# Kernel tuning notes

Measured on AMD Instinct MI355X. Metric: run time of the kernel, lower is better.

The kernel has to match this reference:

```python
import jax, jax.numpy as jnp
import numpy as np

E = 512      # embedding_dim == head_dim
H = 8        # num_heads
F = E * H    # ffn_dim = 4096
B = 2
S = 2048
SCALE = float(np.sqrt(E))


def setup_inputs() -> dict:
    key = jax.random.key(0)
    kx, kq, kk, kv, ko = jax.random.split(key, 5)
    x = jax.random.normal(kx, (B, S, E), dtype=jnp.float32)
    # torch Linear weights: [out_features, in_features], y = x @ W.T
    w_std = 1.0 / np.sqrt(E)
    Wq = jax.random.normal(kq, (F, E), dtype=jnp.float32) * w_std
    Wk = jax.random.normal(kk, (F, E), dtype=jnp.float32) * w_std
    Wv = jax.random.normal(kv, (F, E), dtype=jnp.float32) * w_std
    Wo = jax.random.normal(ko, (E, F), dtype=jnp.float32) * (1.0 / np.sqrt(F))
    # causal mask: 1 where attended, 0 where masked (masked_fill(mask == 0, -inf))
    attn_mask = jnp.tril(jnp.ones((S, S), dtype=jnp.int32))[None, None]  # [1,1,S,S]
    return {"x": x, "attn_mask": attn_mask, "Wq": Wq, "Wk": Wk, "Wv": Wv, "Wo": Wo}


def reference(x, attn_mask, Wq, Wk, Wv, Wo):
    b, s, _ = x.shape
    # projections + split heads: [B,S,F] -> [B,S,H,E]
    q = (x @ Wq.T).reshape(b, s, H, E)
    k = (x @ Wk.T).reshape(b, s, H, E)
    v = (x @ Wv.T).reshape(b, s, H, E)
    # scaled dot-product scores [B,H,S,S]
    scores = jnp.einsum('bqhd,bkhd->bhqk', q, k) / SCALE
    scores = jnp.where(attn_mask == 0, -jnp.inf, scores)
    w = jax.nn.softmax(scores, axis=-1)
    # dropout rate 0.0 (eval) -> identity
    out = jnp.einsum('bhqk,bkhd->bqhd', w, v).reshape(b, s, F)
    return out @ Wo.T  # [B,S,E]
```

## Files before the change

### kernel.cpp

```cpp
#include <hip/hip_runtime.h>
#include <hip/hip_bf16.h>

typedef __attribute__((ext_vector_type(8))) short short8;
typedef __attribute__((ext_vector_type(4))) float f32x4;
typedef __attribute__((ext_vector_type(8))) unsigned short ushort8;

#define LDS_ASYNC16(gsrc, ldst) \
  __builtin_amdgcn_global_load_lds((const __attribute__((address_space(1))) void*)(gsrc), \
                                   (__attribute__((address_space(3))) void*)(ldst), 16, 0, 0)

__device__ __forceinline__ unsigned short f2bf(float f) {
  unsigned int u = __float_as_uint(f);
  unsigned int r = (u + 0x7FFFu + ((u >> 16) & 1u)) >> 16;
  return (unsigned short)r;
}
__device__ __forceinline__ float bf2f(unsigned short h) {
  return __uint_as_float((unsigned int)h << 16);
}

__global__ __launch_bounds__(256) void cast5_f32_bf16(
    const float* __restrict__ i0, const float* __restrict__ i1, const float* __restrict__ i2,
    const float* __restrict__ i3, const float* __restrict__ i4,
    unsigned short* __restrict__ out ) {
  const float* src[5] = {i0, i1, i2, i3, i4};
  int z = blockIdx.z;
  const float* in = src[z];
  size_t i = ((size_t)blockIdx.x * 256 + threadIdx.x) * 8;
  float4 a = *(const float4*)(in + i);
  float4 b = *(const float4*)(in + i + 4);
  ushort8 o;
  o[0] = f2bf(a.x); o[1] = f2bf(a.y); o[2] = f2bf(a.z); o[3] = f2bf(a.w);
  o[4] = f2bf(b.x); o[5] = f2bf(b.y); o[6] = f2bf(b.z); o[7] = f2bf(b.w);
  *(ushort8*)(out + (size_t)z * 2097152 + i) = o;
}

__global__ __launch_bounds__(256) void transpose_v(const unsigned short* __restrict__ V,
                                                   unsigned short* __restrict__ Vt) {
  __shared__ unsigned short t[64][72];
  int slot = blockIdx.z;
  int k0 = blockIdx.x << 6, d0 = blockIdx.y << 6;
  const unsigned short* src = V + (size_t)k0 * 4096 + slot * 512 + d0;
  int rr = threadIdx.x >> 3;
  int cc = (threadIdx.x & 7) << 3;
#pragma unroll
  for (int half = 0; half < 64; half += 32) {
    int r = rr + half;
    ushort8 v = *(const ushort8*)(src + (size_t)r * 4096 + cc);
#pragma unroll
    for (int e = 0; e < 8; ++e) t[cc + e][r] = v[e];
  }
  __syncthreads();
  unsigned short* dst = Vt + ((size_t)slot * 512 + d0) * 2048 + k0;
#pragma unroll
  for (int half = 0; half < 64; half += 32) {
    int d = rr + half;
    *(ushort8*)(dst + (size_t)d * 2048 + cc) = *(const ushort8*)&t[d][cc];
  }
}

__global__ __launch_bounds__(256) void softmax_causal_bf16(unsigned short* __restrict__ S) {
  int row = blockIdx.x;
  int q = row & 2047;
  unsigned short* srow = S + (size_t)row * 2048;
  int n = q + 1;
  int nW = ((q >> 7) + 1) << 7;
  int t = threadIdx.x, wave = t >> 6, lane = t & 63;
  int base = t * 8;
  ushort8 u = *(const ushort8*)(srow + base);
  float vals[8];
  float m = -1e30f;
#pragma unroll
  for (int e = 0; e < 8; ++e) {
    float v = bf2f(u[e]);
    vals[e] = (base + e < n) ? v : -1e30f;
    m = fmaxf(m, vals[e]);
  }
#pragma unroll
  for (int off = 32; off > 0; off >>= 1) m = fmaxf(m, __shfl_xor(m, off, 64));
  __shared__ float red[8];
  if (lane == 0) red[wave] = m;
  __syncthreads();
  m = fmaxf(fmaxf(red[0], red[1]), fmaxf(red[2], red[3]));
  float s = 0.f;
#pragma unroll
  for (int e = 0; e < 8; ++e) {
    float ex = (base + e < n) ? __expf(vals[e] - m) : 0.f;
    vals[e] = ex; s += ex;
  }
#pragma unroll
  for (int off = 32; off > 0; off >>= 1) s += __shfl_xor(s, off, 64);
  if (lane == 0) red[4 + wave] = s;
  __syncthreads();
  s = red[4] + red[5] + red[6] + red[7];
  float inv = 1.0f / s;
  if (base < nW) {
    ushort8 o;
#pragma unroll
    for (int e = 0; e < 8; ++e) o[e] = f2bf(vals[e] * inv);
    *(ushort8*)(srow + base) = o;
  }
}

__global__ __launch_bounds__(256) void reduce_k4(const float4* __restrict__ p,
                                                 float4* __restrict__ out, int n4) {
  int i = blockIdx.x * 256 + threadIdx.x;
  if (i >= n4) return;
  float4 a = p[i], b = p[i + n4], c = p[i + 2 * n4], d = p[i + 3 * n4];
  float4 o;
  o.x = (a.x + b.x) + (c.x + d.x);
  o.y = (a.y + b.y) + (c.y + d.y);
  o.z = (a.z + b.z) + (c.z + d.z);
  o.w = (a.w + b.w) + (c.w + d.w);
  out[i] = o;
}

template<int OUT_F32, int CSKIP, int KCLIP>
__global__ __launch_bounds__(256, 2) void gemm_bt(
    const unsigned short* __restrict__ A, const unsigned short* __restrict__ B,
    void* __restrict__ C, int K, int lda, int ldb, int ldc, int nH,
    long long sAb, long long sAh, long long sBb, long long sBh,
    long long sCb, long long sCh, float scale)
{
  __shared__ unsigned short As[128 * 64];
  __shared__ unsigned short Bs[128 * 64];
  int m0 = blockIdx.y * 128, n0 = blockIdx.x * 128;
  if (CSKIP && n0 > m0) return;
  int z = blockIdx.z;
  int zb = z / nH, zh = z - zb * nH;
  const unsigned short* Ap = A + (size_t)(zb * sAb + zh * sAh);
  const unsigned short* Bp = B + (size_t)(zb * sBb + zh * sBh);
  size_t coff = (size_t)(zb * sCb + zh * sCh);
  int tid = threadIdx.x;
  int wave = tid >> 6, lane = tid & 63;
  int kEnd = KCLIP ? min(K, m0 + 128) : K;

  int wr = (wave >> 1) * 64, wc = (wave & 1) * 64;
  int lr = lane & 15;
  int lkb = (lane >> 4) * 8;

  f32x4 acc[4][4] = {};

  for (int k0 = 0; k0 < kEnd; k0 += 64) {
#pragma unroll
    for (int it = 0; it < 4; ++it) {
      int g = it * 256 + tid;
      int r = g >> 3, c = (g & 7) << 3;
      LDS_ASYNC16(Ap + (size_t)(m0 + r) * lda + (k0 + c), As + (size_t)(it * 256 + wave * 64) * 8);
      LDS_ASYNC16(Bp + (size_t)(n0 + r) * ldb + (k0 + c), Bs + (size_t)(it * 256 + wave * 64) * 8);
    }
    __syncthreads();
#pragma unroll
    for (int kk = 0; kk < 64; kk += 32) {
      short8 a[4], b[4];
#pragma unroll
      for (int i = 0; i < 4; ++i)
        a[i] = *(const short8*)(As + (size_t)(wr + i * 16 + lr) * 64 + kk + lkb);
#pragma unroll
      for (int j = 0; j < 4; ++j)
        b[j] = *(const short8*)(Bs + (size_t)(wc + j * 16 + lr) * 64 + kk + lkb);
#pragma unroll
      for (int i = 0; i < 4; ++i)
#pragma unroll
        for (int j = 0; j < 4; ++j)
          acc[i][j] = __builtin_amdgcn_mfma_f32_16x16x32_bf16(a[i], b[j], acc[i][j], 0, 0, 0);
    }
    __syncthreads();
  }

  int orow = (lane >> 4) * 4, ocol = lane & 15;
#pragma unroll
  for (int i = 0; i < 4; ++i)
#pragma unroll
    for (int j = 0; j < 4; ++j)
#pragma unroll
      for (int r = 0; r < 4; ++r) {
        int row = m0 + wr + i * 16 + orow + r;
        int col = n0 + wc + j * 16 + ocol;
        float v = acc[i][j][r] * scale;
        if (OUT_F32) ((float*)C)[coff + (size_t)row * ldc + col] = v;
        else ((unsigned short*)C)[coff + (size_t)row * ldc + col] = f2bf(v);
      }
}

extern "C" void kernel_launch(void* const* d_in, const int* in_sizes, int n_in,
                              void* d_out, int out_size, void* d_ws, size_t ws_size,
                              hipStream_t stream) {
  const float* x  = (const float*)d_in[0];
  const float* Wq = (const float*)d_in[2];
  const float* Wk = (const float*)d_in[3];
  const float* Wv = (const float*)d_in[4];
  const float* Wo = (const float*)d_in[5];

  if (ws_size < (size_t)188 * (1 << 20)) return;

  char* ws = (char*)d_ws;
  unsigned short* xb   = (unsigned short*)(ws);
  unsigned short* Wob  = (unsigned short*)(ws + (size_t)16  * (1 << 20));
  unsigned short* QKV  = (unsigned short*)(ws + (size_t)20  * (1 << 20));
  unsigned short* Sc   = (unsigned short*)(ws + (size_t)116 * (1 << 20));
  unsigned short* Vt   = (unsigned short*)(ws);
  float*          Pp   = (float*)(ws + (size_t)116 * (1 << 20));

  const int NEw = 4096 * 512;
  const long long NEm = 4096LL * 4096;

  cast5_f32_bf16<<<dim3(1024, 1, 5), 256, 0, stream>>>(x, Wq, Wk, Wv, Wo, xb);

  gemm_bt<0, 0, 0><<<dim3(32, 32, 3), 256, 0, stream>>>(
      xb, xb + NEw, QKV, 512, 512, 512, 4096, 3,
      0LL, 0LL, 0LL, (long long)NEw, 0LL, NEm, 1.0f);

  for (int b = 0; b < 2; ++b) {
    size_t tokOff = (size_t)b * 2048 * 4096;
    const unsigned short* Qb = QKV + tokOff;
    const unsigned short* Kb = QKV + NEm + tokOff;
    const unsigned short* Vb = QKV + 2 * NEm + tokOff;
    unsigned short* AOb = QKV + tokOff;

    gemm_bt<0, 1, 0><<<dim3(16, 16, 8), 256, 0, stream>>>(
        Qb, Kb, Sc, 512, 4096, 4096, 2048, 8,
        0LL, 512LL, 0LL, 512LL, 0LL, 2048LL * 2048, 0.04419417382415922f);

    transpose_v<<<dim3(32, 8, 8), 256, 0, stream>>>(Vb, Vt);

    softmax_causal_bf16<<<dim3(8 * 2048), 256, 0, stream>>>(Sc);

    gemm_bt<0, 0, 1><<<dim3(4, 16, 8), 256, 0, stream>>>(
        Sc, Vt, AOb, 2048, 2048, 2048, 4096, 8,
        0LL, 2048LL * 2048, 0LL, 512LL * 2048, 0LL, 512LL, 1.0f);
  }

  gemm_bt<1, 0, 0><<<dim3(4, 32, 4), 256, 0, stream>>>(
      QKV, Wob, Pp, 1024, 4096, 4096, 512, 4,
      0LL, 1024LL, 0LL, 1024LL, 0LL, 2097152LL, 1.0f);

  reduce_k4<<<dim3(2048), 256, 0, stream>>>((const float4*)Pp, (float4*)d_out, 524288);
}
```

Baseline: 352.8 us.

## Add double-buffered swizzled 256x256 GEMM for QKV projection and scores

Adds a new 512-thread GEMM kernel with 256x256 output tiles. It double-buffers its LDS stages, uses an XOR-swizzled LDS layout to avoid bank conflicts, and raises wave priority around the MFMA bursts. The kernel replaces the 128x128 single-buffered GEMM for the QKV projection and the causal QK^T scores, aiming for more operand reuse and overlap of global loads with compute. The softmax also skips loading score entries beyond the causal write width. In exchange, the large LDS footprint limits occupancy to one block per CU, and the larger tiles waste more work on the causal diagonal and give fewer blocks for the score GEMM.

```diff
diff --git a/kernel.cpp b/kernel.cpp
--- a/kernel.cpp
+++ b/kernel.cpp
@@ -66,7 +66,8 @@
   int nW = ((q >> 7) + 1) << 7;
   int t = threadIdx.x, wave = t >> 6, lane = t & 63;
   int base = t * 8;
-  ushort8 u = *(const ushort8*)(srow + base);
+  ushort8 u = {};
+  if (base < nW) u = *(const ushort8*)(srow + base);
   float vals[8];
   float m = -1e30f;
 #pragma unroll
@@ -112,6 +113,109 @@
   o.z = (a.z + b.z) + (c.z + d.z);
   o.w = (a.w + b.w) + (c.w + d.w);
   out[i] = o;
+}
+
+template<int OUT_F32, int CSKIP>
+__global__ __launch_bounds__(512, 2) void gemm256(
+    const unsigned short* __restrict__ A, const unsigned short* __restrict__ B,
+    void* __restrict__ C, int K, int lda, int ldb, int ldc, int nH,
+    long long sAb, long long sAh, long long sBb, long long sBh,
+    long long sCb, long long sCh, float scale)
+{
+  __shared__ unsigned short As[2][256 * 64];
+  __shared__ unsigned short Bs[2][256 * 64];
+  int m0 = blockIdx.y * 256, n0 = blockIdx.x * 256;
+  if (CSKIP && n0 > m0) return;
+  int z = blockIdx.z;
+  int zb = z / nH, zh = z - zb * nH;
+  const unsigned short* Ap = A + (size_t)(zb * sAb + zh * sAh);
+  const unsigned short* Bp = B + (size_t)(zb * sBb + zh * sBh);
+  size_t coff = (size_t)(zb * sCb + zh * sCh);
+  int tid = threadIdx.x;
+  int wid = tid >> 6, lane = tid & 63;
+  int wm = wid >> 2, wn = wid & 3;
+  int lr = lane & 15, hi = lane >> 4;
+
+  int srow  = (wid << 5) + (lane >> 3);
+  int swcol = ((lane & 7) ^ ((lane >> 3) & 7)) << 3;
+
+#define STAGE256(t_, buf_) do {                                                   \
+    int k0_ = (t_) << 6;                                                          \
+    _Pragma("unroll")                                                             \
+    for (int g_ = 0; g_ < 4; ++g_) {                                              \
+      LDS_ASYNC16(Ap + (size_t)(m0 + srow + g_ * 8) * lda + k0_ + swcol,          \
+                  &As[buf_][(wid * 4 + g_) * 512]);                               \
+      LDS_ASYNC16(Bp + (size_t)(n0 + srow + g_ * 8) * ldb + k0_ + swcol,          \
+                  &Bs[buf_][(wid * 4 + g_) * 512]);                               \
+    }                                                                             \
+  } while (0)
+
+  int s0 = (0 + hi) ^ (lr & 7);
+  int s1 = (4 + hi) ^ (lr & 7);
+
+  int nt = K >> 6;
+  f32x4 acc[8][4] = {};
+
+  STAGE256(0, 0);
+  STAGE256(1, 1);
+  asm volatile("s_waitcnt vmcnt(8)" ::: "memory");
+  __builtin_amdgcn_s_barrier();
+
+  for (int t = 0; t < nt; ++t) {
+    const unsigned short* Ab = As[t & 1];
+    const unsigned short* Bb = Bs[t & 1];
+    short8 bf[4][2];
+#pragma unroll
+    for (int n = 0; n < 4; ++n) {
+      int r = wn * 64 + n * 16 + lr;
+      bf[n][0] = *(const short8*)(Bb + r * 64 + s0 * 8);
+      bf[n][1] = *(const short8*)(Bb + r * 64 + s1 * 8);
+    }
+#pragma unroll
+    for (int p = 0; p < 4; ++p) {
+      short8 af[2][2];
+#pragma unroll
+      for (int mi = 0; mi < 2; ++mi) {
+        int r = wm * 128 + (p * 2 + mi) * 16 + lr;
+        af[mi][0] = *(const short8*)(Ab + r * 64 + s0 * 8);
+        af[mi][1] = *(const short8*)(Ab + r * 64 + s1 * 8);
+      }
+      __builtin_amdgcn_s_setprio(1);
+#pragma unroll
+      for (int kk = 0; kk < 2; ++kk)
+#pragma unroll
+        for (int mi = 0; mi < 2; ++mi)
+#pragma unroll
+          for (int n = 0; n < 4; ++n)
+            acc[p * 2 + mi][n] = __builtin_amdgcn_mfma_f32_16x16x32_bf16(
+                af[mi][kk], bf[n][kk], acc[p * 2 + mi][n], 0, 0, 0);
+      __builtin_amdgcn_s_setprio(0);
+    }
+    if (t + 1 < nt) {
+      __builtin_amdgcn_s_barrier();
+      if (t + 2 < nt) {
+        STAGE256(t + 2, t & 1);
+        asm volatile("s_waitcnt vmcnt(8)" ::: "memory");
+      } else {
+        asm volatile("s_waitcnt vmcnt(0)" ::: "memory");
+      }
+      __builtin_amdgcn_s_barrier();
+    }
+  }
+#undef STAGE256
+
+#pragma unroll
+  for (int m = 0; m < 8; ++m)
+#pragma unroll
+    for (int n = 0; n < 4; ++n)
+#pragma unroll
+      for (int r = 0; r < 4; ++r) {
+        int row = m0 + wm * 128 + m * 16 + hi * 4 + r;
+        int col = n0 + wn * 64 + n * 16 + lr;
+        float v = acc[m][n][r] * scale;
+        if (OUT_F32) ((float*)C)[coff + (size_t)row * ldc + col] = v;
+        else ((unsigned short*)C)[coff + (size_t)row * ldc + col] = f2bf(v);
+      }
 }
 
 template<int OUT_F32, int CSKIP, int KCLIP>
@@ -206,7 +310,7 @@
 
   cast5_f32_bf16<<<dim3(1024, 1, 5), 256, 0, stream>>>(x, Wq, Wk, Wv, Wo, xb);
 
-  gemm_bt<0, 0, 0><<<dim3(32, 32, 3), 256, 0, stream>>>(
+  gemm256<0, 0><<<dim3(16, 16, 3), 512, 0, stream>>>(
       xb, xb + NEw, QKV, 512, 512, 512, 4096, 3,
       0LL, 0LL, 0LL, (long long)NEw, 0LL, NEm, 1.0f);
 
@@ -217,7 +321,7 @@
     const unsigned short* Vb = QKV + 2 * NEm + tokOff;
     unsigned short* AOb = QKV + tokOff;
 
-    gemm_bt<0, 1, 0><<<dim3(16, 16, 8), 256, 0, stream>>>(
+    gemm256<0, 1><<<dim3(8, 8, 8), 512, 0, stream>>>(
         Qb, Kb, Sc, 512, 4096, 4096, 2048, 8,
         0LL, 512LL, 0LL, 512LL, 0LL, 2048LL * 2048, 0.04419417382415922f);
 
```

After: 352.9 us. No clear change (+0.0%).

## Add 256x256 eight-wave pipelined GEMM for QKV projection and QK scores

Applied to the files above, without the earlier changes.

Introduces a new 512-thread GEMM kernel with 256x256 tiles, a four-slot LDS ring of 32-wide K halves, swizzled LDS layout, interleaved async global-to-LDS staging with explicit vmcnt waits, barriers and setprio around MFMA bursts. It replaces the 128x128 GEMM for the QKV projection and the causal score GEMM, aiming to hide load latency and raise MFMA utilisation. The softmax also skips reading masked-out tail chunks of each row. The larger tile means fewer blocks and coarser causal skipping, which wastes more work on the diagonal and lowers occupancy.

```diff
diff --git a/kernel.cpp b/kernel.cpp
--- a/kernel.cpp
+++ b/kernel.cpp
@@ -21,7 +21,7 @@
 __global__ __launch_bounds__(256) void cast5_f32_bf16(
     const float* __restrict__ i0, const float* __restrict__ i1, const float* __restrict__ i2,
     const float* __restrict__ i3, const float* __restrict__ i4,
-    unsigned short* __restrict__ out ) {
+    unsigned short* __restrict__ out) {
   const float* src[5] = {i0, i1, i2, i3, i4};
   int z = blockIdx.z;
   const float* in = src[z];
@@ -66,7 +66,8 @@
   int nW = ((q >> 7) + 1) << 7;
   int t = threadIdx.x, wave = t >> 6, lane = t & 63;
   int base = t * 8;
-  ushort8 u = *(const ushort8*)(srow + base);
+  ushort8 u = {};
+  if (base < nW) u = *(const ushort8*)(srow + base);
   float vals[8];
   float m = -1e30f;
 #pragma unroll
@@ -112,6 +113,112 @@
   o.z = (a.z + b.z) + (c.z + d.z);
   o.w = (a.w + b.w) + (c.w + d.w);
   out[i] = o;
+}
+
+#define STG(Ptr, rb, ld, t_, kh_, ldsbase)                                            \
+  do {                                                                                \
+    LDS_ASYNC16((Ptr) + (size_t)((rb) + r0) * (ld) + (t_) * 64 + (kh_) * 32 + cs0,    \
+                (ldsbase) + (size_t)tid * 8);                                         \
+    LDS_ASYNC16((Ptr) + (size_t)((rb) + r0 + 128) * (ld) + (t_) * 64 + (kh_) * 32 + cs0, \
+                (ldsbase) + (size_t)tid * 8 + 4096);                                  \
+  } while (0)
+
+#define PAIRQ(qq, I, STEADY)                                                          \
+  {                                                                                   \
+    const unsigned short* Au = As + (qq) * 8192;                                      \
+    const unsigned short* Bu = Bs + (qq) * 8192;                                      \
+    short8 af[8], bfr[2];                                                             \
+    _Pragma("unroll") for (int j = 0; j < 8; ++j)                                     \
+      af[j] = *(const short8*)(Au + (wm * 128 + j * 16 + lr) * 32 + sA);              \
+    _Pragma("unroll") for (int j2 = 0; j2 < 2; ++j2)                                  \
+      bfr[j2] = *(const short8*)(Bu + (wn * 64 + j2 * 16 + lr) * 32 + sA);            \
+    if ((qq) == 0)      STG(Ap, m0, lda, 2 * (I) + 1, 1, As + 3 * 8192);              \
+    else if (STEADY) {                                                                \
+      if ((qq) == 1)      STG(Ap, m0, lda, 2 * (I) + 2, 0, As + 0 * 8192);            \
+      else if ((qq) == 2) STG(Ap, m0, lda, 2 * (I) + 2, 1, As + 1 * 8192);            \
+      else                STG(Ap, m0, lda, 2 * (I) + 3, 0, As + 2 * 8192);            \
+    }                                                                                 \
+    __builtin_amdgcn_s_barrier();                                                     \
+    __builtin_amdgcn_s_setprio(1);                                                    \
+    _Pragma("unroll") for (int j = 0; j < 8; ++j)                                     \
+      _Pragma("unroll") for (int j2 = 0; j2 < 2; ++j2)                                \
+        acc[j][j2] = __builtin_amdgcn_mfma_f32_16x16x32_bf16(af[j], bfr[j2], acc[j][j2], 0, 0, 0); \
+    __builtin_amdgcn_s_setprio(0);                                                    \
+    __builtin_amdgcn_s_barrier();                                                     \
+    _Pragma("unroll") for (int j2 = 0; j2 < 2; ++j2)                                  \
+      bfr[j2] = *(const short8*)(Bu + (wn * 64 + (2 + j2) * 16 + lr) * 32 + sA);      \
+    if ((qq) == 0)      STG(Bp, n0, ldb, 2 * (I) + 1, 1, Bs + 3 * 8192);              \
+    else if (STEADY) {                                                                \
+      if ((qq) == 1)      STG(Bp, n0, ldb, 2 * (I) + 2, 0, Bs + 0 * 8192);            \
+      else if ((qq) == 2) STG(Bp, n0, ldb, 2 * (I) + 2, 1, Bs + 1 * 8192);            \
+      else                STG(Bp, n0, ldb, 2 * (I) + 3, 0, Bs + 2 * 8192);            \
+    }                                                                                 \
+    if (STEADY) { asm volatile("s_waitcnt vmcnt(8)" ::: "memory"); }                  \
+    else if ((qq) == 0) { asm volatile("s_waitcnt vmcnt(8)" ::: "memory"); }          \
+    else if ((qq) == 1) { asm volatile("s_waitcnt vmcnt(4)" ::: "memory"); }          \
+    else if ((qq) == 2) { asm volatile("s_waitcnt vmcnt(0)" ::: "memory"); }          \
+    __builtin_amdgcn_s_barrier();                                                     \
+    __builtin_amdgcn_s_setprio(1);                                                    \
+    _Pragma("unroll") for (int j = 0; j < 8; ++j)                                     \
+      _Pragma("unroll") for (int j2 = 0; j2 < 2; ++j2)                                \
+        acc[j][2 + j2] = __builtin_amdgcn_mfma_f32_16x16x32_bf16(af[j], bfr[j2], acc[j][2 + j2], 0, 0, 0); \
+    __builtin_amdgcn_s_setprio(0);                                                    \
+    __builtin_amdgcn_s_barrier();                                                     \
+  }
+
+template<int OUT_F32, int CSKIP>
+__global__ __launch_bounds__(512, 2) void gemm8p(
+    const unsigned short* __restrict__ A, const unsigned short* __restrict__ B,
+    void* __restrict__ C, int K, int lda, int ldb, int ldc, int nH,
+    long long sAb, long long sAh, long long sBb, long long sBh,
+    long long sCb, long long sCh, float scale)
+{
+  __shared__ unsigned short As[4 * 8192];
+  __shared__ unsigned short Bs[4 * 8192];
+  int m0 = blockIdx.y * 256, n0 = blockIdx.x * 256;
+  if (CSKIP && n0 > m0) return;
+  int z = blockIdx.z;
+  int zb = z / nH, zh = z - zb * nH;
+  const unsigned short* Ap = A + (size_t)(zb * sAb + zh * sAh);
+  const unsigned short* Bp = B + (size_t)(zb * sBb + zh * sBh);
+  size_t coff = (size_t)(zb * sCb + zh * sCh);
+  int tid = threadIdx.x;
+  int wid = tid >> 6, lane = tid & 63;
+  int wm = wid >> 2, wn = wid & 3;
+  int lr = lane & 15, hi = lane >> 4;
+  int sA = ((hi ^ (lr & 3)) << 3);
+  int r0 = tid >> 2;
+  int cs0 = (((tid & 3) ^ (r0 & 3)) << 3);
+
+  int nt = K >> 6, ni = nt >> 1;
+  f32x4 acc[8][4] = {};
+
+  STG(Ap, m0, lda, 0, 0, As + 0 * 8192);  STG(Bp, n0, ldb, 0, 0, Bs + 0 * 8192);
+  STG(Ap, m0, lda, 0, 1, As + 1 * 8192);  STG(Bp, n0, ldb, 0, 1, Bs + 1 * 8192);
+  STG(Ap, m0, lda, 1, 0, As + 2 * 8192);  STG(Bp, n0, ldb, 1, 0, Bs + 2 * 8192);
+  asm volatile("s_waitcnt vmcnt(8)" ::: "memory");
+  __builtin_amdgcn_s_barrier();
+
+  for (int i = 0; i < ni - 1; ++i) {
+    PAIRQ(0, i, 1) PAIRQ(1, i, 1) PAIRQ(2, i, 1) PAIRQ(3, i, 1)
+  }
+  {
+    int i = ni - 1;
+    PAIRQ(0, i, 0) PAIRQ(1, i, 0) PAIRQ(2, i, 0) PAIRQ(3, i, 0)
+  }
+
+#pragma unroll
+  for (int m = 0; m < 8; ++m)
+#pragma unroll
+    for (int n = 0; n < 4; ++n)
+#pragma unroll
+      for (int r = 0; r < 4; ++r) {
+        int row = m0 + wm * 128 + m * 16 + hi * 4 + r;
+        int col = n0 + wn * 64 + n * 16 + lr;
+        float v = acc[m][n][r] * scale;
+        if (OUT_F32) ((float*)C)[coff + (size_t)row * ldc + col] = v;
+        else ((unsigned short*)C)[coff + (size_t)row * ldc + col] = f2bf(v);
+      }
 }
 
 template<int OUT_F32, int CSKIP, int KCLIP>
@@ -206,7 +313,7 @@
 
   cast5_f32_bf16<<<dim3(1024, 1, 5), 256, 0, stream>>>(x, Wq, Wk, Wv, Wo, xb);
 
-  gemm_bt<0, 0, 0><<<dim3(32, 32, 3), 256, 0, stream>>>(
+  gemm8p<0, 0><<<dim3(16, 16, 3), 512, 0, stream>>>(
       xb, xb + NEw, QKV, 512, 512, 512, 4096, 3,
       0LL, 0LL, 0LL, (long long)NEw, 0LL, NEm, 1.0f);
 
@@ -217,7 +324,7 @@
     const unsigned short* Vb = QKV + 2 * NEm + tokOff;
     unsigned short* AOb = QKV + tokOff;
 
-    gemm_bt<0, 1, 0><<<dim3(16, 16, 8), 256, 0, stream>>>(
+    gemm8p<0, 1><<<dim3(8, 8, 8), 512, 0, stream>>>(
         Qb, Kb, Sc, 512, 4096, 4096, 2048, 8,
         0LL, 512LL, 0LL, 512LL, 0LL, 2048LL * 2048, 0.04419417382415922f);
 
```

Result: slower. 362.1 us (+2.6%).

## Add 256x256 multi-stage pipelined GEMM for QKV and score projections

Applied to the files above, without the earlier changes.

Introduces a new 512-thread GEMM kernel with 256x256 tiles, a 4-slot LDS ring buffer with three stages of async global-to-LDS prefetch, swizzled LDS layout to avoid bank conflicts, and s_setprio around MFMA blocks. It is used for the QKV projection and the QK^T score GEMM in place of the 128x128 single-buffered kernel, aiming to overlap memory loads with compute and improve reuse. The softmax also skips loading score entries beyond the causal write window. Larger tiles reduce block count (coarser causal skipping on the score GEMM) and use heavy LDS/register resources, which may limit occupancy.

```diff
diff --git a/kernel.cpp b/kernel.cpp
--- a/kernel.cpp
+++ b/kernel.cpp
@@ -21,7 +21,7 @@
 __global__ __launch_bounds__(256) void cast5_f32_bf16(
     const float* __restrict__ i0, const float* __restrict__ i1, const float* __restrict__ i2,
     const float* __restrict__ i3, const float* __restrict__ i4,
-    unsigned short* __restrict__ out ) {
+    unsigned short* __restrict__ out) {
   const float* src[5] = {i0, i1, i2, i3, i4};
   int z = blockIdx.z;
   const float* in = src[z];
@@ -66,7 +66,8 @@
   int nW = ((q >> 7) + 1) << 7;
   int t = threadIdx.x, wave = t >> 6, lane = t & 63;
   int base = t * 8;
-  ushort8 u = *(const ushort8*)(srow + base);
+  ushort8 u = {};
+  if (base < nW) u = *(const ushort8*)(srow + base);
   float vals[8];
   float m = -1e30f;
 #pragma unroll
@@ -112,6 +113,89 @@
   o.z = (a.z + b.z) + (c.z + d.z);
   o.w = (a.w + b.w) + (c.w + d.w);
   out[i] = o;
+}
+
+#define STGU(u_)                                                                   \
+  do {                                                                             \
+    int kb_ = (u_) * 32;                                                           \
+    unsigned short* Ad_ = AsBase + ((u_) & 3) * 8192 + tid * 8;                    \
+    unsigned short* Bd_ = BsBase + ((u_) & 3) * 8192 + tid * 8;                    \
+    LDS_ASYNC16(Ap + (size_t)(m0 + r0) * lda + kb_ + cs0, Ad_);                    \
+    LDS_ASYNC16(Bp + (size_t)(n0 + r0) * ldb + kb_ + cs0, Bd_);                    \
+    LDS_ASYNC16(Ap + (size_t)(m0 + r0 + 128) * lda + kb_ + cs0, Ad_ + 4096);       \
+    LDS_ASYNC16(Bp + (size_t)(n0 + r0 + 128) * ldb + kb_ + cs0, Bd_ + 4096);       \
+  } while (0)
+
+#define UNITPH(u_, STAGE_, WAITOP_)                                                \
+  {                                                                                \
+    const unsigned short* Au = AsBase + ((u_) & 3) * 8192;                         \
+    const unsigned short* Bu = BsBase + ((u_) & 3) * 8192;                         \
+    short8 af[8], bf[4];                                                           \
+    _Pragma("unroll") for (int j = 0; j < 8; ++j)                                  \
+      af[j] = *(const short8*)(Au + (wm * 128 + j * 16 + lr) * 32 + sA);           \
+    _Pragma("unroll") for (int j = 0; j < 4; ++j)                                  \
+      bf[j] = *(const short8*)(Bu + (wn * 64 + j * 16 + lr) * 32 + sA);            \
+    if (STAGE_) STGU((u_) + 3);                                                    \
+    __builtin_amdgcn_s_barrier();                                                  \
+    __builtin_amdgcn_s_setprio(1);                                                 \
+    _Pragma("unroll") for (int j = 0; j < 8; ++j)                                  \
+      _Pragma("unroll") for (int j2 = 0; j2 < 4; ++j2)                             \
+        acc[j][j2] = __builtin_amdgcn_mfma_f32_16x16x32_bf16(af[j], bf[j2],        \
+                                                             acc[j][j2], 0, 0, 0); \
+    __builtin_amdgcn_s_setprio(0);                                                 \
+    WAITOP_;                                                                       \
+    __builtin_amdgcn_s_barrier();                                                  \
+  }
+
+template<int OUT_F32, int CSKIP>
+__global__ __launch_bounds__(512, 2) void gemm8p(
+    const unsigned short* __restrict__ A, const unsigned short* __restrict__ B,
+    void* __restrict__ C, int K, int lda, int ldb, int ldc, int nH,
+    long long sAb, long long sAh, long long sBb, long long sBh,
+    long long sCb, long long sCh, float scale)
+{
+  __shared__ unsigned short AsBase[4 * 8192];
+  __shared__ unsigned short BsBase[4 * 8192];
+  int m0 = blockIdx.y * 256, n0 = blockIdx.x * 256;
+  if (CSKIP && n0 > m0) return;
+  int z = blockIdx.z;
+  int zb = z / nH, zh = z - zb * nH;
+  const unsigned short* Ap = A + (size_t)(zb * sAb + zh * sAh);
+  const unsigned short* Bp = B + (size_t)(zb * sBb + zh * sBh);
+  size_t coff = (size_t)(zb * sCb + zh * sCh);
+  int tid = threadIdx.x;
+  int wid = tid >> 6, lane = tid & 63;
+  int wm = wid >> 2, wn = wid & 3;
+  int lr = lane & 15, hi = lane >> 4;
+  int sA  = (hi ^ ((lr >> 1) & 3)) << 3;
+  int r0  = tid >> 2;
+  int cs0 = ((tid & 3) ^ ((r0 >> 1) & 3)) << 3;
+
+  int N = K >> 5;
+  f32x4 acc[8][4] = {};
+
+  STGU(0); STGU(1); STGU(2);
+  asm volatile("s_waitcnt vmcnt(8)" ::: "memory");
+  __builtin_amdgcn_s_barrier();
+
+  for (int u = 0; u + 3 < N; ++u)
+    UNITPH(u, 1, asm volatile("s_waitcnt vmcnt(8)" ::: "memory"))
+  UNITPH(N - 3, 0, asm volatile("s_waitcnt vmcnt(4)" ::: "memory"))
+  UNITPH(N - 2, 0, asm volatile("s_waitcnt vmcnt(0)" ::: "memory"))
+  UNITPH(N - 1, 0, )
+
+#pragma unroll
+  for (int m = 0; m < 8; ++m)
+#pragma unroll
+    for (int n = 0; n < 4; ++n)
+#pragma unroll
+      for (int r = 0; r < 4; ++r) {
+        int row = m0 + wm * 128 + m * 16 + hi * 4 + r;
+        int col = n0 + wn * 64 + n * 16 + lr;
+        float v = acc[m][n][r] * scale;
+        if (OUT_F32) ((float*)C)[coff + (size_t)row * ldc + col] = v;
+        else ((unsigned short*)C)[coff + (size_t)row * ldc + col] = f2bf(v);
+      }
 }
 
 template<int OUT_F32, int CSKIP, int KCLIP>
@@ -206,7 +290,7 @@
 
   cast5_f32_bf16<<<dim3(1024, 1, 5), 256, 0, stream>>>(x, Wq, Wk, Wv, Wo, xb);
 
-  gemm_bt<0, 0, 0><<<dim3(32, 32, 3), 256, 0, stream>>>(
+  gemm8p<0, 0><<<dim3(16, 16, 3), 512, 0, stream>>>(
       xb, xb + NEw, QKV, 512, 512, 512, 4096, 3,
       0LL, 0LL, 0LL, (long long)NEw, 0LL, NEm, 1.0f);
 
@@ -217,7 +301,7 @@
     const unsigned short* Vb = QKV + 2 * NEm + tokOff;
     unsigned short* AOb = QKV + tokOff;
 
-    gemm_bt<0, 1, 0><<<dim3(16, 16, 8), 256, 0, stream>>>(
+    gemm8p<0, 1><<<dim3(8, 8, 8), 512, 0, stream>>>(
         Qb, Kb, Sc, 512, 4096, 4096, 2048, 8,
         0LL, 512LL, 0LL, 512LL, 0LL, 2048LL * 2048, 0.04419417382415922f);
 
```

Result: no change. 346.4 us (-1.8%).
